# Kernel optimization log

Measured on AMD Instinct MI355X. Metric: run time of the kernel, lower is better.

The kernel has to match this reference:

```python
import jax, jax.numpy as jnp
import numpy as np


def setup_inputs() -> dict:
    key = jax.random.key(0)
    k1, k2 = jax.random.split(key, 2)
    B, C, H, W = 64, 1024, 32, 32
    feature_maps = jax.random.normal(k1, (B, C, H, W), dtype=jnp.float32)
    # 1x1 conv (C -> 1) is just a channel contraction: weight [C], bias [1]
    conv_w = jax.random.normal(k2, (C,), dtype=jnp.float32) * 0.02
    conv_b = jnp.zeros((1,), dtype=jnp.float32)
    M = 768  # int(H * W * drop_rate) = int(1024 * 0.75)
    return {"feature_maps": feature_maps, "conv_w": conv_w, "conv_b": conv_b, "M": M}


def reference(feature_maps, conv_w, conv_b, M):
    # Training-mode ADL forward.
    B, C, H, W = feature_maps.shape
    # 1x1 conv to a single channel + sigmoid -> attention map [B, H, W]
    attn = jax.nn.sigmoid(jnp.einsum('bchw,c->bhw', feature_maps, conv_w) + conv_b[0])
    attn_flat = attn.reshape(B, H * W)
    # drop the top-M most attended spatial locations
    _, topk_idx = jax.lax.top_k(attn_flat, M)            # [B, M]
    drop_mask = jnp.ones_like(attn_flat)
    drop_mask = drop_mask.at[jnp.arange(B)[:, None], topk_idx].set(0.0)
    drop_mask = drop_mask.reshape(B, 1, H, W)
    dropped = feature_maps * drop_mask                   # broadcast over channels
    return dropped, attn.reshape(B, 1, H, W)
```

## Files before the change

kernel.cpp:

```cpp
#include <hip/hip_runtime.h>

typedef float f32x4 __attribute__((ext_vector_type(4)));

#define NB 64
#define NC 1024
#define HW 1024
#define HW4 256
#define CCH 16
#define CPC (NC / CCH)
#define CGRP 16
#define CPG (NC / CGRP)

__global__ void __launch_bounds__(256)
adl_gemv(const float* __restrict__ fm,
         const float* __restrict__ w,
         float* __restrict__ partial) {
    const int cg = blockIdx.x;
    const int b  = blockIdx.y;
    const int t  = threadIdx.x;
    const f32x4* fm4 = (const f32x4*)fm;
    const int cbase = cg * CPC;
    size_t base = ((size_t)(b * NC + cbase)) * HW4 + t;
    f32x4 acc = {0.f, 0.f, 0.f, 0.f};
    #pragma unroll 8
    for (int ci = 0; ci < CPC; ++ci) {
        acc += fm4[base] * w[cbase + ci];
        base += HW4;
    }
    ((f32x4*)partial)[((size_t)(cg * NB + b)) * HW4 + t] = acc;
}

__global__ void __launch_bounds__(256)
adl_topk_mask(const float* __restrict__ partial,
              const float* __restrict__ conv_b,
              const int* __restrict__ Mptr,
              float* __restrict__ attn_out,
              float* __restrict__ mask) {
    __shared__ f32x4 s_sh4[HW4];
    float* s_sh = (float*)s_sh4;
    const int slice = blockIdx.x;
    const int b     = blockIdx.y;
    const int tid   = threadIdx.x;
    const float bias = conv_b[0];
    #pragma unroll
    for (int q = 0; q < 4; ++q) {
        const int t = q * 256 + tid;
        float s = bias;
        #pragma unroll 8
        for (int k = 0; k < CCH; ++k)
            s += partial[((size_t)(k * NB + b)) * HW + t];
        s_sh[t] = s;
    }
    __syncthreads();
    const int t = slice * 256 + tid;
    const float sv = s_sh[t];
    const int M = *Mptr;
    int r = 0;
    #pragma unroll 4
    for (int j4 = 0; j4 < HW4; ++j4) {
        const f32x4 v = s_sh4[j4];
        const int j = j4 * 4;
        r += (v.x > sv) || (v.x == sv && (j + 0) < t);
        r += (v.y > sv) || (v.y == sv && (j + 1) < t);
        r += (v.z > sv) || (v.z == sv && (j + 2) < t);
        r += (v.w > sv) || (v.w == sv && (j + 3) < t);
    }
    attn_out[(size_t)b * HW + t] = 1.0f / (1.0f + expf(-sv));
    mask[(size_t)b * HW + t] = (r < M) ? 0.0f : 1.0f;
}

__global__ void __launch_bounds__(256)
adl_apply(const float* __restrict__ fm,
          const float* __restrict__ mask,
          float* __restrict__ out) {
    const int cg = blockIdx.x;
    const int b  = blockIdx.y;
    const int t  = threadIdx.x;
    const f32x4* fm4   = (const f32x4*)fm;
    const f32x4* mask4 = (const f32x4*)mask;
    f32x4* out4        = (f32x4*)out;
    const f32x4 m = mask4[b * HW4 + t];
    size_t base = ((size_t)(b * NC + cg * CPG)) * HW4 + t;
    #pragma unroll 4
    for (int ci = 0; ci < CPG; ++ci) {
        const f32x4 v = __builtin_nontemporal_load(&fm4[base]);
        __builtin_nontemporal_store(v * m, &out4[base]);
        base += HW4;
    }
}

extern "C" void kernel_launch(void* const* d_in, const int* in_sizes, int n_in,
                              void* d_out, int out_size, void* d_ws, size_t ws_size,
                              hipStream_t stream) {
    const float* fm   = (const float*)d_in[0];
    const float* w    = (const float*)d_in[1];
    const float* bias = (const float*)d_in[2];
    const int*   Mptr = (const int*)d_in[3];

    float* out      = (float*)d_out;
    float* attn_out = out + (size_t)NB * NC * HW;

    float* partial = (float*)d_ws;
    float* mask    = partial + (size_t)CCH * NB * HW;

    adl_gemv<<<dim3(CCH, NB), 256, 0, stream>>>(fm, w, partial);
    adl_topk_mask<<<dim3(4, NB), 256, 0, stream>>>(partial, bias, Mptr, attn_out, mask);
    adl_apply<<<dim3(CGRP, NB), 256, 0, stream>>>(fm, mask, out);
}
```

Measured before the change: 161.3 us.

## Fuse gemv, top-k mask and apply into one cooperative kernel with grid syncs

Replaces the three separate launches with a single cooperative kernel that computes the channel-contraction partials, grid-syncs, computes the attention and rank-based drop mask, grid-syncs again, then applies the mask. It is meant to remove inter-kernel launch gaps and tail effects, and it caches the conv weights in shared memory. In exchange it adds two grid-wide barriers and requires all 1024 blocks to be co-resident, falling back to the old three-kernel path if the cooperative launch fails.

```diff
diff --git a/kernel.cpp b/kernel.cpp
--- a/kernel.cpp
+++ b/kernel.cpp
@@ -1,4 +1,7 @@
 #include <hip/hip_runtime.h>
+#include <hip/hip_cooperative_groups.h>
+
+namespace coop = cooperative_groups;
 
 typedef float f32x4 __attribute__((ext_vector_type(4)));
 
@@ -8,47 +11,113 @@
 #define HW4 256
 #define CCH 16
 #define CPC (NC / CCH)
-#define CGRP 16
-#define CPG (NC / CGRP)
+
+__global__ void __launch_bounds__(256, 4)
+adl_fused(const float* __restrict__ fm,
+          const float* __restrict__ w,
+          const float* __restrict__ conv_b,
+          const int* __restrict__ Mptr,
+          float* __restrict__ out,
+          float* __restrict__ attn_out,
+          float* __restrict__ partial,
+          float* __restrict__ mask) {
+    const int bid = blockIdx.x;
+    const int b   = bid & (NB - 1);
+    const int cg  = bid >> 6;
+    const int t   = threadIdx.x;
+
+    __shared__ float wsh[CPC];
+    __shared__ f32x4 s_sh4[HW4];
+    float* s_sh = (float*)s_sh4;
+
+    if (t < CPC) wsh[t] = w[cg * CPC + t];
+    __syncthreads();
+    {
+        const f32x4* fm4 = (const f32x4*)fm;
+        size_t base = ((size_t)(b * NC + cg * CPC)) * HW4 + t;
+        f32x4 acc = {0.f, 0.f, 0.f, 0.f};
+        #pragma unroll 8
+        for (int ci = 0; ci < CPC; ++ci) {
+            acc += fm4[base] * wsh[ci];
+            base += HW4;
+        }
+        ((f32x4*)partial)[((size_t)(cg * NB + b)) * HW4 + t] = acc;
+    }
+    coop::this_grid().sync();
+
+    if (cg < 4) {
+        const int slice = cg;
+        const float bias = conv_b[0];
+        #pragma unroll
+        for (int q = 0; q < 4; ++q) {
+            const int tt = q * 256 + t;
+            float s = bias;
+            #pragma unroll 8
+            for (int k = 0; k < CCH; ++k)
+                s += partial[((size_t)(k * NB + b)) * HW + tt];
+            s_sh[tt] = s;
+        }
+        __syncthreads();
+        const int tt = slice * 256 + t;
+        const float sv = s_sh[tt];
+        const int M = *Mptr;
+        int r = 0;
+        #pragma unroll 4
+        for (int j4 = 0; j4 < HW4; ++j4) {
+            const f32x4 v = s_sh4[j4];
+            const int j = j4 * 4;
+            r += (v.x > sv) || (v.x == sv && (j + 0) < tt);
+            r += (v.y > sv) || (v.y == sv && (j + 1) < tt);
+            r += (v.z > sv) || (v.z == sv && (j + 2) < tt);
+            r += (v.w > sv) || (v.w == sv && (j + 3) < tt);
+        }
+        attn_out[(size_t)b * HW + tt] = 1.0f / (1.0f + expf(-sv));
+        mask[(size_t)b * HW + tt] = (r < M) ? 0.0f : 1.0f;
+    }
+    coop::this_grid().sync();
+
+    {
+        const f32x4* fm4   = (const f32x4*)fm;
+        const f32x4* mask4 = (const f32x4*)mask;
+        f32x4* out4        = (f32x4*)out;
+        const f32x4 m = mask4[b * HW4 + t];
+        size_t base = ((size_t)(b * NC + cg * CPC)) * HW4 + t;
+        #pragma unroll 4
+        for (int ci = 0; ci < CPC; ++ci) {
+            const f32x4 v = __builtin_nontemporal_load(&fm4[base]);
+            __builtin_nontemporal_store(v * m, &out4[base]);
+            base += HW4;
+        }
+    }
+}
 
 __global__ void __launch_bounds__(256)
-adl_gemv(const float* __restrict__ fm,
-         const float* __restrict__ w,
+adl_gemv(const float* __restrict__ fm, const float* __restrict__ w,
          float* __restrict__ partial) {
-    const int cg = blockIdx.x;
-    const int b  = blockIdx.y;
-    const int t  = threadIdx.x;
+    const int cg = blockIdx.x, b = blockIdx.y, t = threadIdx.x;
     const f32x4* fm4 = (const f32x4*)fm;
     const int cbase = cg * CPC;
     size_t base = ((size_t)(b * NC + cbase)) * HW4 + t;
     f32x4 acc = {0.f, 0.f, 0.f, 0.f};
     #pragma unroll 8
-    for (int ci = 0; ci < CPC; ++ci) {
-        acc += fm4[base] * w[cbase + ci];
-        base += HW4;
-    }
+    for (int ci = 0; ci < CPC; ++ci) { acc += fm4[base] * w[cbase + ci]; base += HW4; }
     ((f32x4*)partial)[((size_t)(cg * NB + b)) * HW4 + t] = acc;
 }
 
 __global__ void __launch_bounds__(256)
-adl_topk_mask(const float* __restrict__ partial,
-              const float* __restrict__ conv_b,
-              const int* __restrict__ Mptr,
-              float* __restrict__ attn_out,
+adl_topk_mask(const float* __restrict__ partial, const float* __restrict__ conv_b,
+              const int* __restrict__ Mptr, float* __restrict__ attn_out,
               float* __restrict__ mask) {
     __shared__ f32x4 s_sh4[HW4];
     float* s_sh = (float*)s_sh4;
-    const int slice = blockIdx.x;
-    const int b     = blockIdx.y;
-    const int tid   = threadIdx.x;
+    const int slice = blockIdx.x, b = blockIdx.y, tid = threadIdx.x;
     const float bias = conv_b[0];
     #pragma unroll
     for (int q = 0; q < 4; ++q) {
         const int t = q * 256 + tid;
         float s = bias;
         #pragma unroll 8
-        for (int k = 0; k < CCH; ++k)
-            s += partial[((size_t)(k * NB + b)) * HW + t];
+        for (int k = 0; k < CCH; ++k) s += partial[((size_t)(k * NB + b)) * HW + t];
         s_sh[t] = s;
     }
     __syncthreads();
@@ -70,19 +139,16 @@
 }
 
 __global__ void __launch_bounds__(256)
-adl_apply(const float* __restrict__ fm,
-          const float* __restrict__ mask,
+adl_apply(const float* __restrict__ fm, const float* __restrict__ mask,
           float* __restrict__ out) {
-    const int cg = blockIdx.x;
-    const int b  = blockIdx.y;
-    const int t  = threadIdx.x;
-    const f32x4* fm4   = (const f32x4*)fm;
+    const int cg = blockIdx.x, b = blockIdx.y, t = threadIdx.x;
+    const f32x4* fm4 = (const f32x4*)fm;
     const f32x4* mask4 = (const f32x4*)mask;
-    f32x4* out4        = (f32x4*)out;
+    f32x4* out4 = (f32x4*)out;
     const f32x4 m = mask4[b * HW4 + t];
-    size_t base = ((size_t)(b * NC + cg * CPG)) * HW4 + t;
+    size_t base = ((size_t)(b * NC + cg * CPC)) * HW4 + t;
     #pragma unroll 4
-    for (int ci = 0; ci < CPG; ++ci) {
+    for (int ci = 0; ci < CPC; ++ci) {
         const f32x4 v = __builtin_nontemporal_load(&fm4[base]);
         __builtin_nontemporal_store(v * m, &out4[base]);
         base += HW4;
@@ -103,7 +169,14 @@
     float* partial = (float*)d_ws;
     float* mask    = partial + (size_t)CCH * NB * HW;
 
-    adl_gemv<<<dim3(CCH, NB), 256, 0, stream>>>(fm, w, partial);
-    adl_topk_mask<<<dim3(4, NB), 256, 0, stream>>>(partial, bias, Mptr, attn_out, mask);
-    adl_apply<<<dim3(CGRP, NB), 256, 0, stream>>>(fm, mask, out);
+    void* args[] = {(void*)&fm, (void*)&w, (void*)&bias, (void*)&Mptr,
+                    (void*)&out, (void*)&attn_out, (void*)&partial, (void*)&mask};
+    hipError_t err = hipLaunchCooperativeKernel((const void*)adl_fused,
+                                                dim3(CCH * NB), dim3(256),
+                                                args, 0, stream);
+    if (err != hipSuccess) {
+        adl_gemv<<<dim3(CCH, NB), 256, 0, stream>>>(fm, w, partial);
+        adl_topk_mask<<<dim3(4, NB), 256, 0, stream>>>(partial, bias, Mptr, attn_out, mask);
+        adl_apply<<<dim3(CCH, NB), 256, 0, stream>>>(fm, mask, out);
+    }
 }
```

Result: slower. 384.9 us (+138.6%).

## Fuse gemv, top-k mask and apply into one persistent kernel with spin barriers

Applied to the files above, without the earlier changes.

Merges the three kernels into a single launch of 1024 blocks. Each block computes a channel-chunk partial dot product, then a per-batch atomic counter acts as a barrier so four blocks can compute the top-k rank mask and the rest spin-wait before applying it to the same channel chunk. The intent is to remove launch gaps and to re-read the chunk of feature maps each block just streamed while it may still be in cache. It relies on all 1024 blocks being co-resident, since spin-waiting could otherwise deadlock, and it adds an extra flag-init launch.

```diff
diff --git a/kernel.cpp b/kernel.cpp
--- a/kernel.cpp
+++ b/kernel.cpp
@@ -8,84 +8,108 @@
 #define HW4 256
 #define CCH 16
 #define CPC (NC / CCH)
-#define CGRP 16
-#define CPG (NC / CGRP)
+#define FPAD 32
 
-__global__ void __launch_bounds__(256)
-adl_gemv(const float* __restrict__ fm,
-         const float* __restrict__ w,
-         float* __restrict__ partial) {
-    const int cg = blockIdx.x;
-    const int b  = blockIdx.y;
-    const int t  = threadIdx.x;
-    const f32x4* fm4 = (const f32x4*)fm;
-    const int cbase = cg * CPC;
-    size_t base = ((size_t)(b * NC + cbase)) * HW4 + t;
-    f32x4 acc = {0.f, 0.f, 0.f, 0.f};
-    #pragma unroll 8
-    for (int ci = 0; ci < CPC; ++ci) {
-        acc += fm4[base] * w[cbase + ci];
-        base += HW4;
-    }
-    ((f32x4*)partial)[((size_t)(cg * NB + b)) * HW4 + t] = acc;
+__global__ void adl_init_flags(int* __restrict__ flags) {
+    flags[threadIdx.x * FPAD] = 0;
 }
 
-__global__ void __launch_bounds__(256)
-adl_topk_mask(const float* __restrict__ partial,
-              const float* __restrict__ conv_b,
-              const int* __restrict__ Mptr,
-              float* __restrict__ attn_out,
-              float* __restrict__ mask) {
+__global__ void __launch_bounds__(256, 4)
+adl_fused_spin(const float* __restrict__ fm,
+               const float* __restrict__ w,
+               const float* __restrict__ conv_b,
+               const int* __restrict__ Mptr,
+               float* __restrict__ out,
+               float* __restrict__ attn_out,
+               float* __restrict__ partial,
+               float* __restrict__ mask,
+               int* __restrict__ cnt,
+               int* __restrict__ cnt2) {
+    const int bid = blockIdx.x;
+    const int b   = bid & (NB - 1);
+    const int cg  = bid >> 6;
+    const int t   = threadIdx.x;
+
+    __shared__ float wsh[CPC];
     __shared__ f32x4 s_sh4[HW4];
     float* s_sh = (float*)s_sh4;
-    const int slice = blockIdx.x;
-    const int b     = blockIdx.y;
-    const int tid   = threadIdx.x;
-    const float bias = conv_b[0];
-    #pragma unroll
-    for (int q = 0; q < 4; ++q) {
-        const int t = q * 256 + tid;
-        float s = bias;
+
+    if (t < CPC) wsh[t] = w[cg * CPC + t];
+    __syncthreads();
+    const f32x4* fm4 = (const f32x4*)fm;
+    {
+        size_t base = ((size_t)(b * NC + cg * CPC)) * HW4 + t;
+        f32x4 acc = {0.f, 0.f, 0.f, 0.f};
         #pragma unroll 8
-        for (int k = 0; k < CCH; ++k)
-            s += partial[((size_t)(k * NB + b)) * HW + t];
-        s_sh[t] = s;
+        for (int ci = 0; ci < CPC; ++ci) {
+            acc += fm4[base] * wsh[ci];
+            base += HW4;
+        }
+        ((f32x4*)partial)[((size_t)(cg * NB + b)) * HW4 + t] = acc;
+    }
+    __threadfence();
+    __syncthreads();
+    if (t == 0)
+        __hip_atomic_fetch_add(&cnt[b * FPAD], 1, __ATOMIC_RELEASE,
+                               __HIP_MEMORY_SCOPE_AGENT);
+
+    if (cg < 4) {
+        if (t == 0) {
+            while (__hip_atomic_load(&cnt[b * FPAD], __ATOMIC_ACQUIRE,
+                                     __HIP_MEMORY_SCOPE_AGENT) < CCH)
+                __builtin_amdgcn_s_sleep(4);
+        }
+        __syncthreads();
+        const float bias = conv_b[0];
+        #pragma unroll
+        for (int q = 0; q < 4; ++q) {
+            const int tt = q * 256 + t;
+            float s = bias;
+            #pragma unroll
+            for (int k = 0; k < CCH; ++k)
+                s += partial[((size_t)(k * NB + b)) * HW + tt];
+            s_sh[tt] = s;
+        }
+        __syncthreads();
+        const int tt = cg * 256 + t;
+        const float sv = s_sh[tt];
+        const int M = *Mptr;
+        attn_out[(size_t)b * HW + tt] = 1.0f / (1.0f + expf(-sv));
+        int r = 0;
+        #pragma unroll 4
+        for (int j4 = 0; j4 < HW4; ++j4) {
+            const f32x4 v = s_sh4[j4];
+            const int j = j4 * 4;
+            r += (v.x > sv) || (v.x == sv && (j + 0) < tt);
+            r += (v.y > sv) || (v.y == sv && (j + 1) < tt);
+            r += (v.z > sv) || (v.z == sv && (j + 2) < tt);
+            r += (v.w > sv) || (v.w == sv && (j + 3) < tt);
+        }
+        mask[(size_t)b * HW + tt] = (r < M) ? 0.0f : 1.0f;
+        __threadfence();
+        __syncthreads();
+        if (t == 0)
+            __hip_atomic_fetch_add(&cnt2[b * FPAD], 1, __ATOMIC_RELEASE,
+                                   __HIP_MEMORY_SCOPE_AGENT);
+    }
+
+    if (t == 0) {
+        while (__hip_atomic_load(&cnt2[b * FPAD], __ATOMIC_ACQUIRE,
+                                 __HIP_MEMORY_SCOPE_AGENT) < 4)
+            __builtin_amdgcn_s_sleep(4);
     }
     __syncthreads();
-    const int t = slice * 256 + tid;
-    const float sv = s_sh[t];
-    const int M = *Mptr;
-    int r = 0;
-    #pragma unroll 4
-    for (int j4 = 0; j4 < HW4; ++j4) {
-        const f32x4 v = s_sh4[j4];
-        const int j = j4 * 4;
-        r += (v.x > sv) || (v.x == sv && (j + 0) < t);
-        r += (v.y > sv) || (v.y == sv && (j + 1) < t);
-        r += (v.z > sv) || (v.z == sv && (j + 2) < t);
-        r += (v.w > sv) || (v.w == sv && (j + 3) < t);
-    }
-    attn_out[(size_t)b * HW + t] = 1.0f / (1.0f + expf(-sv));
-    mask[(size_t)b * HW + t] = (r < M) ? 0.0f : 1.0f;
-}
-
-__global__ void __launch_bounds__(256)
-adl_apply(const float* __restrict__ fm,
-          const float* __restrict__ mask,
-          float* __restrict__ out) {
-    const int cg = blockIdx.x;
-    const int b  = blockIdx.y;
-    const int t  = threadIdx.x;
-    const f32x4* fm4   = (const f32x4*)fm;
-    const f32x4* mask4 = (const f32x4*)mask;
-    f32x4* out4        = (f32x4*)out;
-    const f32x4 m = mask4[b * HW4 + t];
-    size_t base = ((size_t)(b * NC + cg * CPG)) * HW4 + t;
-    #pragma unroll 4
-    for (int ci = 0; ci < CPG; ++ci) {
-        const f32x4 v = __builtin_nontemporal_load(&fm4[base]);
-        __builtin_nontemporal_store(v * m, &out4[base]);
-        base += HW4;
+    {
+        const f32x4* mask4 = (const f32x4*)mask;
+        f32x4* out4        = (f32x4*)out;
+        const f32x4 m = mask4[b * HW4 + t];
+        size_t base = ((size_t)(b * NC + cg * CPC)) * HW4 + t;
+        #pragma unroll 4
+        for (int ci = 0; ci < CPC; ++ci) {
+            const f32x4 v = __builtin_nontemporal_load(&fm4[base]);
+            __builtin_nontemporal_store(v * m, &out4[base]);
+            base += HW4;
+        }
     }
 }
 
@@ -102,8 +126,11 @@
 
     float* partial = (float*)d_ws;
     float* mask    = partial + (size_t)CCH * NB * HW;
+    int*   cnt     = (int*)(mask + (size_t)NB * HW);
+    int*   cnt2    = cnt + NB * FPAD;
 
-    adl_gemv<<<dim3(CCH, NB), 256, 0, stream>>>(fm, w, partial);
-    adl_topk_mask<<<dim3(4, NB), 256, 0, stream>>>(partial, bias, Mptr, attn_out, mask);
-    adl_apply<<<dim3(CGRP, NB), 256, 0, stream>>>(fm, mask, out);
+    adl_init_flags<<<1, 2 * NB, 0, stream>>>(cnt);
+    adl_fused_spin<<<CCH * NB, 256, 0, stream>>>(fm, w, bias, Mptr, out,
+                                                 attn_out, partial, mask,
+                                                 cnt, cnt2);
 }
```

Measured after the change: 445.6 us. 2.76x slower.
